# Kernel optimization log

Hardware: AMD Instinct MI355X
Metric: run time of the kernel (lower is better)

The kernel has to match this reference:

```python
import jax, jax.numpy as jnp
import numpy as np
import math

N = 256          # DFT size
B = 262144       # number of frames (batch)


def _dft_matrix(n):
    # W[r, c] = exp(-2j*pi/n) ** (r*c)
    rc = np.outer(np.arange(n), np.arange(n))
    W = np.exp(-2j * np.pi * rc / n)
    return W


def setup_inputs() -> dict:
    key = jax.random.key(0)
    k1, k2 = jax.random.split(key)
    x_real = jax.random.normal(k1, (B, N), dtype=jnp.float32)
    x_imag = jax.random.normal(k2, (B, N), dtype=jnp.float32)
    W = _dft_matrix(N)
    W_real = jnp.asarray(np.real(W), dtype=jnp.float32)
    W_imag = jnp.asarray(np.imag(W), dtype=jnp.float32)
    return {"x_real": x_real, "x_imag": x_imag, "W_real": W_real, "W_imag": W_imag}


def reference(x_real, x_imag, W_real, W_imag):
    # complex_mul via 4 real matmuls, then normal=True epilogue scale 1/sqrt(n)
    real = jnp.matmul(x_real, W_real) - jnp.matmul(x_imag, W_imag)
    imag = jnp.matmul(x_real, W_imag) + jnp.matmul(x_imag, W_real)
    scale = 1.0 / math.sqrt(N)
    return (real * scale, imag * scale)
```

## Files before the change

kernel.cpp:

```cpp
#include <hip/hip_runtime.h>
#include <math.h>

#define FS 264

__device__ __forceinline__ void dft16(float* xr, float* xi) {
  constexpr float TWR[10] = {1.f, 0.9238795325f, 0.7071067812f, 0.3826834324f, 0.f,
                             -0.3826834324f, -0.7071067812f, -0.9238795325f, -1.f,
                             -0.9238795325f};
  constexpr float TWI[10] = {0.f, -0.3826834324f, -0.7071067812f, -0.9238795325f, -1.f,
                             -0.9238795325f, -0.7071067812f, -0.3826834324f, 0.f,
                             0.3826834324f};
  float yr[16], yi[16];
#pragma unroll
  for (int b = 0; b < 4; ++b) {
    float x0r = xr[b],      x0i = xi[b];
    float x1r = xr[b + 4],  x1i = xi[b + 4];
    float x2r = xr[b + 8],  x2i = xi[b + 8];
    float x3r = xr[b + 12], x3i = xi[b + 12];
    float t0r = x0r + x2r, t0i = x0i + x2i;
    float t1r = x0r - x2r, t1i = x0i - x2i;
    float t2r = x1r + x3r, t2i = x1i + x3i;
    float t3r = x1r - x3r, t3i = x1i - x3i;
    yr[0 + b]  = t0r + t2r;  yi[0 + b]  = t0i + t2i;
    yr[8 + b]  = t0r - t2r;  yi[8 + b]  = t0i - t2i;
    yr[4 + b]  = t1r + t3i;  yi[4 + b]  = t1i - t3r;
    yr[12 + b] = t1r - t3i;  yi[12 + b] = t1i + t3r;
  }
#pragma unroll
  for (int c = 0; c < 4; ++c) {
    float zr[4], zi[4];
#pragma unroll
    for (int b = 0; b < 4; ++b) {
      const int k = b * c;
      float ar = yr[c * 4 + b], ai = yi[c * 4 + b];
      zr[b] = ar * TWR[k] - ai * TWI[k];
      zi[b] = ar * TWI[k] + ai * TWR[k];
    }
    float t0r = zr[0] + zr[2], t0i = zi[0] + zi[2];
    float t1r = zr[0] - zr[2], t1i = zi[0] - zi[2];
    float t2r = zr[1] + zr[3], t2i = zi[1] + zi[3];
    float t3r = zr[1] - zr[3], t3i = zi[1] - zi[3];
    xr[c]      = t0r + t2r;  xi[c]      = t0i + t2i;
    xr[c + 8]  = t0r - t2r;  xi[c + 8]  = t0i - t2i;
    xr[c + 4]  = t1r + t3i;  xi[c + 4]  = t1i - t3r;
    xr[c + 12] = t1r - t3i;  xi[c + 12] = t1i + t3r;
  }
}

__global__ __launch_bounds__(256, 4) void dft256_kernel(
    const float* __restrict__ xr, const float* __restrict__ xi,
    float* __restrict__ out, size_t half) {
  __shared__ __align__(16) float s[16 * FS];
  const int t = threadIdx.x;
  const int f = t >> 4;
  const int b = t & 15;
  const size_t frame = (size_t)blockIdx.x * 16 + f;

  const float* gr = xr + frame * 256 + b;
  const float* gi = xi + frame * 256 + b;
  float vr[16], vi[16];
#pragma unroll
  for (int a = 0; a < 16; ++a) {
    vr[a] = __builtin_nontemporal_load(gr + a * 16);
    vi[a] = __builtin_nontemporal_load(gi + a * 16);
  }

  dft16(vr, vi);

  float swb, cwb;
  __sincosf(-6.283185307179586f * (float)b * (1.0f / 256.0f), &swb, &cwb);
  float twr = 1.f, twi = 0.f;
#pragma unroll
  for (int c = 0; c < 16; ++c) {
    float ar = vr[c], ai = vi[c];
    vr[c] = ar * twr - ai * twi;
    vi[c] = ar * twi + ai * twr;
    float ntr = twr * cwb - twi * swb;
    twi = twr * swb + twi * cwb;
    twr = ntr;
  }

  const int fb = f * FS;
  const int rbase = fb + b * 16;
  float ur[16], ui[16];
#pragma unroll
  for (int c = 0; c < 16; ++c) s[fb + c * 16 + b] = vr[c];
  asm volatile("s_waitcnt lgkmcnt(0)" ::: "memory");
#pragma unroll
  for (int j = 0; j < 4; ++j) {
    float4 q = *(const float4*)&s[rbase + 4 * j];
    ur[4 * j + 0] = q.x; ur[4 * j + 1] = q.y;
    ur[4 * j + 2] = q.z; ur[4 * j + 3] = q.w;
  }
  asm volatile("s_waitcnt lgkmcnt(0)" ::: "memory");
#pragma unroll
  for (int c = 0; c < 16; ++c) s[fb + c * 16 + b] = vi[c];
  asm volatile("s_waitcnt lgkmcnt(0)" ::: "memory");
#pragma unroll
  for (int j = 0; j < 4; ++j) {
    float4 q = *(const float4*)&s[rbase + 4 * j];
    ui[4 * j + 0] = q.x; ui[4 * j + 1] = q.y;
    ui[4 * j + 2] = q.z; ui[4 * j + 3] = q.w;
  }

  dft16(ur, ui);

  float* go_r = out + frame * 256 + b;
  float* go_i = out + half + frame * 256 + b;
#pragma unroll
  for (int d = 0; d < 16; ++d) {
    __builtin_nontemporal_store(ur[d] * 0.0625f, go_r + d * 16);
    __builtin_nontemporal_store(ui[d] * 0.0625f, go_i + d * 16);
  }
}

extern "C" void kernel_launch(void* const* d_in, const int* in_sizes, int n_in,
                              void* d_out, int out_size, void* d_ws, size_t ws_size,
                              hipStream_t stream) {
  const float* xr = (const float*)d_in[0];
  const float* xi = (const float*)d_in[1];
  float* out = (float*)d_out;
  const size_t half = (size_t)in_sizes[0];
  const int blocks = (int)(half / 4096);
  dft256_kernel<<<blocks, 256, 0, stream>>>(xr, xi, out, half);
}
```

Measured before the change: 848.7 us.

## Stage global loads and stores through LDS to use float4 coalesced accesses

Replaces the strided scalar nontemporal global loads and stores with wave-contiguous float4 accesses. The data is transposed through shared memory, so each thread still receives its 16-stride elements for the radix-16 stages. This cuts the number of memory instructions and makes global transactions wider. In exchange it adds LDS round-trips, more waitcnt fences, and register pressure. It also drops the nontemporal hints.

Result: no change. 834.8 us (-1.6%).

```diff
diff --git a/kernel.cpp b/kernel.cpp
--- a/kernel.cpp
+++ b/kernel.cpp
@@ -47,23 +47,42 @@
   }
 }
 
+#define LFENCE asm volatile("s_waitcnt lgkmcnt(0)" ::: "memory")
+
 __global__ __launch_bounds__(256, 4) void dft256_kernel(
     const float* __restrict__ xr, const float* __restrict__ xi,
     float* __restrict__ out, size_t half) {
   __shared__ __align__(16) float s[16 * FS];
   const int t = threadIdx.x;
+  const int w = t >> 6;
+  const int l = t & 63;
   const int f = t >> 4;
   const int b = t & 15;
-  const size_t frame = (size_t)blockIdx.x * 16 + f;
+  const int fb = f * FS;
+  const int io_slot = (w * 4) * FS + (l >> 2) * 16 + (l & 3) * 4;
+  const size_t blk4 = (size_t)blockIdx.x * 1024;
+  const size_t wb4 = blk4 + (size_t)w * 256 + l;
 
-  const float* gr = xr + frame * 256 + b;
-  const float* gi = xi + frame * 256 + b;
+  const float4* xr4 = (const float4*)xr;
+  const float4* xi4 = (const float4*)xi;
+  float4 R[4], I[4];
+#pragma unroll
+  for (int i = 0; i < 4; ++i) R[i] = xr4[wb4 + (size_t)i * 64];
+#pragma unroll
+  for (int i = 0; i < 4; ++i) I[i] = xi4[wb4 + (size_t)i * 64];
+
   float vr[16], vi[16];
 #pragma unroll
-  for (int a = 0; a < 16; ++a) {
-    vr[a] = __builtin_nontemporal_load(gr + a * 16);
-    vi[a] = __builtin_nontemporal_load(gi + a * 16);
-  }
+  for (int i = 0; i < 4; ++i) *(float4*)&s[io_slot + i * FS] = R[i];
+  LFENCE;
+#pragma unroll
+  for (int a = 0; a < 16; ++a) vr[a] = s[fb + a * 16 + b];
+  LFENCE;
+#pragma unroll
+  for (int i = 0; i < 4; ++i) *(float4*)&s[io_slot + i * FS] = I[i];
+  LFENCE;
+#pragma unroll
+  for (int a = 0; a < 16; ++a) vi[a] = s[fb + a * 16 + b];
 
   dft16(vr, vi);
 
@@ -80,38 +99,48 @@
     twr = ntr;
   }
 
-  const int fb = f * FS;
-  const int rbase = fb + b * 16;
   float ur[16], ui[16];
+  LFENCE;
 #pragma unroll
   for (int c = 0; c < 16; ++c) s[fb + c * 16 + b] = vr[c];
-  asm volatile("s_waitcnt lgkmcnt(0)" ::: "memory");
+  LFENCE;
 #pragma unroll
   for (int j = 0; j < 4; ++j) {
-    float4 q = *(const float4*)&s[rbase + 4 * j];
+    float4 q = *(const float4*)&s[fb + b * 16 + 4 * j];
     ur[4 * j + 0] = q.x; ur[4 * j + 1] = q.y;
     ur[4 * j + 2] = q.z; ur[4 * j + 3] = q.w;
   }
-  asm volatile("s_waitcnt lgkmcnt(0)" ::: "memory");
+  LFENCE;
 #pragma unroll
   for (int c = 0; c < 16; ++c) s[fb + c * 16 + b] = vi[c];
-  asm volatile("s_waitcnt lgkmcnt(0)" ::: "memory");
+  LFENCE;
 #pragma unroll
   for (int j = 0; j < 4; ++j) {
-    float4 q = *(const float4*)&s[rbase + 4 * j];
+    float4 q = *(const float4*)&s[fb + b * 16 + 4 * j];
     ui[4 * j + 0] = q.x; ui[4 * j + 1] = q.y;
     ui[4 * j + 2] = q.z; ui[4 * j + 3] = q.w;
   }
 
   dft16(ur, ui);
 
-  float* go_r = out + frame * 256 + b;
-  float* go_i = out + half + frame * 256 + b;
+  float4* outr4 = (float4*)out;
+  float4* outi4 = (float4*)(out + half);
+  LFENCE;
 #pragma unroll
-  for (int d = 0; d < 16; ++d) {
-    __builtin_nontemporal_store(ur[d] * 0.0625f, go_r + d * 16);
-    __builtin_nontemporal_store(ui[d] * 0.0625f, go_i + d * 16);
-  }
+  for (int d = 0; d < 16; ++d) s[fb + d * 16 + b] = ur[d] * 0.0625f;
+  LFENCE;
+#pragma unroll
+  for (int i = 0; i < 4; ++i) R[i] = *(const float4*)&s[io_slot + i * FS];
+#pragma unroll
+  for (int i = 0; i < 4; ++i) outr4[wb4 + (size_t)i * 64] = R[i];
+  LFENCE;
+#pragma unroll
+  for (int d = 0; d < 16; ++d) s[fb + d * 16 + b] = ui[d] * 0.0625f;
+  LFENCE;
+#pragma unroll
+  for (int i = 0; i < 4; ++i) I[i] = *(const float4*)&s[io_slot + i * FS];
+#pragma unroll
+  for (int i = 0; i < 4; ++i) outi4[wb4 + (size_t)i * 64] = I[i];
 }
 
 extern "C" void kernel_launch(void* const* d_in, const int* in_sizes, int n_in,
```
